# Optimization experiments

Hardware: AMD Instinct MI355X
Metric: run time of the kernel (lower is better)

Reference implementation:

```python
import jax, jax.numpy as jnp
import numpy as np

DIM = 256
HEADS = 4
B, N = 2, 4096
NEG = -1e9
EPS = 1e-5


def setup_inputs() -> dict:
    key = jax.random.key(0)
    ks = jax.random.split(key, 12)
    s = 0.02
    inp = {
        "x": jax.random.normal(ks[0], (B, N, DIM), dtype=jnp.float32),
        "adj": jax.random.randint(ks[1], (B, N, N), 0, 2, dtype=jnp.int32),
        "Wq": jax.random.normal(ks[2], (DIM, DIM), dtype=jnp.float32) * s,
        "bq": jnp.zeros((DIM,), jnp.float32),
        "Wk": jax.random.normal(ks[3], (DIM, DIM), dtype=jnp.float32) * s,
        "bk": jnp.zeros((DIM,), jnp.float32),
        "Wv": jax.random.normal(ks[4], (DIM, DIM), dtype=jnp.float32) * s,
        "bv": jnp.zeros((DIM,), jnp.float32),
        "Wo": jax.random.normal(ks[5], (DIM, DIM), dtype=jnp.float32) * s,
        "bo": jnp.zeros((DIM,), jnp.float32),
        "gamma": jnp.ones((DIM,), jnp.float32),
        "beta": jnp.zeros((DIM,), jnp.float32),
    }
    return inp


def reference(x, adj, Wq, bq, Wk, bk, Wv, bv, Wo, bo, gamma, beta):
    Bx, Nx, C = x.shape
    H = HEADS
    D = C // H
    scale = D ** (-0.5)
    # torch Linear: y = x @ W.T + b
    def proj(W, b):
        return (x @ W.T + b).reshape(Bx, Nx, H, D).transpose(0, 2, 1, 3)  # [B,H,N,D]
    q = proj(Wq, bq)
    k = proj(Wk, bk)
    v = proj(Wv, bv)
    attn = jnp.einsum("bhnd,bhmd->bhnm", q, k) * scale          # [B,H,N,N]
    attn = jnp.where(adj[:, None, :, :] == 0, NEG, attn)
    attn = jax.nn.softmax(attn, axis=-1)
    # dropout omitted (eval mode / deterministic reference)
    out = jnp.einsum("bhnm,bhmd->bhnd", attn, v)                # [B,H,N,D]
    out = out.transpose(0, 2, 1, 3).reshape(Bx, Nx, C)
    out = out @ Wo.T + bo
    mu = jnp.mean(out, axis=-1, keepdims=True)
    var = jnp.var(out, axis=-1, keepdims=True)
    return (out - mu) * jax.lax.rsqrt(var + EPS) * gamma + beta
```

## Files before the change

kernel.cpp:

```cpp
#include <hip/hip_runtime.h>
#include <stdint.h>

#define CDIM 256
#define HEADS 4
#define HD 64
#define NB 2
#define NN 4096

typedef unsigned short u16;
typedef unsigned char u8;
typedef unsigned long long u64;
typedef __attribute__((ext_vector_type(8))) short short8;
typedef __attribute__((ext_vector_type(4))) float f32x4;
typedef __attribute__((ext_vector_type(16))) float f32x16;

#define QSCALE 0.1803368801111244f

__device__ __forceinline__ u16 f2bf(float f) {
  union { float f; unsigned u; } v; v.f = f;
  return (u16)((v.u + 0x7fffu + ((v.u >> 16) & 1u)) >> 16);
}
__device__ __forceinline__ float bf2f(u16 u) {
  union { unsigned u; float f; } v; v.u = ((unsigned)u) << 16; return v.f;
}
__device__ __forceinline__ short8 fragf32(const float* p) {
  float4 a = reinterpret_cast<const float4*>(p)[0];
  float4 b = reinterpret_cast<const float4*>(p)[1];
  short8 h;
  h[0] = (short)f2bf(a.x); h[1] = (short)f2bf(a.y);
  h[2] = (short)f2bf(a.z); h[3] = (short)f2bf(a.w);
  h[4] = (short)f2bf(b.x); h[5] = (short)f2bf(b.y);
  h[6] = (short)f2bf(b.z); h[7] = (short)f2bf(b.w);
  return h;
}
__device__ __forceinline__ f32x16 zero16() {
  f32x16 z;
#pragma unroll
  for (int i = 0; i < 16; ++i) z[i] = 0.f;
  return z;
}
__device__ __forceinline__ unsigned cvt_pk_bf16(float lo, float hi) {
  unsigned r;
  asm("v_cvt_pk_bf16_f32 %0, %1, %2" : "=v"(r) : "v"(lo), "v"(hi));
  return r;
}
__device__ __forceinline__ void permlane32_swap(unsigned& a, unsigned& b) {
  asm("v_permlane32_swap_b32 %0, %1" : "+v"(a), "+v"(b));
}

__global__ __launch_bounds__(256) void prep(
    const int* __restrict__ adj, u8* __restrict__ bmb,
    const float* __restrict__ Wq, const float* __restrict__ Wk,
    const float* __restrict__ Wv, const float* __restrict__ Wo,
    u16* __restrict__ Wqb, u16* __restrict__ Wkb,
    u16* __restrict__ Wvb, u16* __restrict__ Wob) {
  const int blk = blockIdx.x;
  if (blk < 4096) {
    const int wave = threadIdx.x >> 6, lane = threadIdx.x & 63;
    const int c0 = blk * 16 + wave * 4;
#pragma unroll
    for (int it = 0; it < 4; ++it) {
      int c = c0 + it;
      int row = c >> 3, kb = (c & 7) * 512;
      const int* src = adj + (size_t)row * 4096 + kb + lane * 8;
      uint4 a = *reinterpret_cast<const uint4*>(src);
      uint4 b = *reinterpret_cast<const uint4*>(src + 4);
      unsigned byte = 0;
      byte |= (a.x != 0) ? 1u : 0u;
      byte |= (a.y != 0) ? 2u : 0u;
      byte |= (a.z != 0) ? 4u : 0u;
      byte |= (a.w != 0) ? 8u : 0u;
      byte |= (b.x != 0) ? 16u : 0u;
      byte |= (b.y != 0) ? 32u : 0u;
      byte |= (b.z != 0) ? 64u : 0u;
      byte |= (b.w != 0) ? 128u : 0u;
      bmb[(size_t)row * 512 + (c & 7) * 64 + lane] = (u8)byte;
    }
  } else {
    size_t base = ((size_t)(blk - 4096) * 256 + threadIdx.x) * 8;
    int w = (int)(base >> 16);
    size_t lo = base & 65535;
    const float* src;
    u16* dst;
    if (w == 0)      { src = Wq + lo; dst = Wqb + lo; }
    else if (w == 1) { src = Wk + lo; dst = Wkb + lo; }
    else if (w == 2) { src = Wv + lo; dst = Wvb + lo; }
    else             { src = Wo + lo; dst = Wob + lo; }
    *reinterpret_cast<short8*>(dst) = fragf32(src);
  }
}

__global__ __launch_bounds__(256) void qkv_gemm(
    const float* __restrict__ x,
    const u16* __restrict__ Wqb, const u16* __restrict__ Wkb,
    const u16* __restrict__ Wvb,
    const float* __restrict__ bq, const float* __restrict__ bk,
    const float* __restrict__ bv,
    u16* __restrict__ Qb, u16* __restrict__ Kb, u16* __restrict__ Vtb) {
  const int tid = threadIdx.x, w = tid >> 6, lane = tid & 63;
  const int quad = lane >> 4, l15 = lane & 15;
  const int tok0 = blockIdx.x * 16;
  const int b = tok0 >> 12, nl = tok0 & 4095;
  const int ym = blockIdx.y;

  f32x4 acc[4];
#pragma unroll
  for (int i = 0; i < 4; ++i) acc[i] = (f32x4){0.f, 0.f, 0.f, 0.f};

  if (ym < 2) {
    const u16* Wb = (ym == 0) ? Wqb : Wkb;
    const float* bias = (ym == 0) ? bq : bk;
    const float scale = (ym == 0) ? QSCALE : 1.0f;
    u16* outp = (ym == 0) ? Qb : Kb;
#pragma unroll
    for (int ks = 0; ks < 8; ++ks) {
      short8 af = fragf32(x + (size_t)(tok0 + l15) * 256 + ks * 32 + quad * 8);
#pragma unroll
      for (int ns = 0; ns < 4; ++ns) {
        short8 bf = *reinterpret_cast<const short8*>(
            &Wb[(size_t)(w * 64 + ns * 16 + l15) * 256 + ks * 32 + quad * 8]);
        acc[ns] = __builtin_amdgcn_mfma_f32_16x16x32_bf16(af, bf, acc[ns], 0, 0, 0);
      }
    }
#pragma unroll
    for (int ns = 0; ns < 4; ++ns) {
      int d = ns * 16 + l15;
      float bb = bias[w * 64 + d];
#pragma unroll
      for (int r = 0; r < 4; ++r) {
        int tok = nl + quad * 4 + r;
        outp[((size_t)(b * HEADS + w) * NN + tok) * HD + d] =
            f2bf((acc[ns][r] + bb) * scale);
      }
    }
  } else {
#pragma unroll
    for (int ks = 0; ks < 8; ++ks) {
      short8 xf = fragf32(x + (size_t)(tok0 + l15) * 256 + ks * 32 + quad * 8);
#pragma unroll
      for (int ms = 0; ms < 4; ++ms) {
        short8 wf = *reinterpret_cast<const short8*>(
            &Wvb[(size_t)(w * 64 + ms * 16 + l15) * 256 + ks * 32 + quad * 8]);
        acc[ms] = __builtin_amdgcn_mfma_f32_16x16x32_bf16(wf, xf, acc[ms], 0, 0, 0);
      }
    }
#pragma unroll
    for (int ms = 0; ms < 4; ++ms) {
#pragma unroll
      for (int r = 0; r < 4; ++r) {
        int d = ms * 16 + quad * 4 + r;
        float bb = bv[w * 64 + d];
        Vtb[((size_t)((b * HEADS + w) * HD + d)) * NN + nl + l15] =
            f2bf(acc[ms][r] + bb);
      }
    }
  }
}

__global__ __launch_bounds__(256) void attn_mfma(
    const u16* __restrict__ Qb, const u16* __restrict__ Kb,
    const u16* __restrict__ Vtb, const u64* __restrict__ bm,
    u16* __restrict__ Opb, float* __restrict__ Lp) {
  __shared__ __align__(16) u16 KVs[2 * 8192];

  const int tid = threadIdx.x;
  const int wave = tid >> 6, lane = tid & 63;
  const int h5 = lane >> 5, l31 = lane & 31, l7 = lane & 7;
  const int bh = blockIdx.y, b = bh >> 2, h = bh & 3;
  const int q0 = blockIdx.x * 128 + wave * 32;
  const int half = blockIdx.z;
  const int key0 = half * 2048;

  const u16* qr = Qb + ((size_t)bh * NN + q0 + l31) * HD + h5 * 8;
  const short8 qf0 = *reinterpret_cast<const short8*>(qr);
  const short8 qf1 = *reinterpret_cast<const short8*>(qr + 16);
  const short8 qf2 = *reinterpret_cast<const short8*>(qr + 32);
  const short8 qf3 = *reinterpret_cast<const short8*>(qr + 48);

  short8 ones;
#pragma unroll
  for (int i = 0; i < 8; ++i) ones[i] = (short)0x3F80;

  f32x16 Oacc0 = zero16(), Oacc1 = zero16(), Oli = zero16();

  int sdk[4];
#pragma unroll
  for (int j = 0; j < 4; ++j) sdk[j] = ((2 * j + h5) ^ l7) << 3;

  const int srow = tid >> 2;
  const int wbu0 = ((((tid & 3) * 2)     ^ (srow & 7)) << 3) + srow * 64;
  const int wbu1 = ((((tid & 3) * 2 + 1) ^ (srow & 7)) << 3) + srow * 64;

  const u16* kbase = Kb + (size_t)bh * NN * HD + (size_t)key0 * HD;
  const u16* vbase = Vtb + (size_t)bh * HD * NN + key0;
  const u64* bmr = bm + ((size_t)b * NN + q0 + l31) * 64 + half * 32;

  uint4 k0, k1, v0, v1;
  {
    const uint4* kp = reinterpret_cast<const uint4*>(kbase) + tid * 2;
    k0 = kp[0]; k1 = kp[1];
    const u16* vp = vbase + (size_t)srow * NN + (tid & 3) * 16;
    v0 = *reinterpret_cast<const uint4*>(vp);
    v1 = *reinterpret_cast<const uint4*>(vp + 8);
  }
  *reinterpret_cast<uint4*>(&KVs[wbu0]) = k0;
  *reinterpret_cast<uint4*>(&KVs[wbu1]) = k1;
  *reinterpret_cast<uint4*>(&KVs[4096 + wbu0]) = v0;
  *reinterpret_cast<uint4*>(&KVs[4096 + wbu1]) = v1;
  {
    const uint4* kp = reinterpret_cast<const uint4*>(kbase + 4096) + tid * 2;
    k0 = kp[0]; k1 = kp[1];
    const u16* vp = vbase + (size_t)srow * NN + 64 + (tid & 3) * 16;
    v0 = *reinterpret_cast<const uint4*>(vp);
    v1 = *reinterpret_cast<const uint4*>(vp + 8);
  }
  u64 amc = bmr[0];

  for (int mt = 0; mt < 32; ++mt) {
    __syncthreads();
    const u64 am = amc;
    if (mt + 1 < 32) amc = bmr[mt + 1];
    const int cb = (mt & 1) * 8192;

    f32x16 s0 = zero16(), s1 = zero16();
#pragma unroll
    for (int dk = 0; dk < 4; ++dk) {
      short8 a0 = *reinterpret_cast<const short8*>(&KVs[cb + l31 * 64 + sdk[dk]]);
      short8 a1 = *reinterpret_cast<const short8*>(&KVs[cb + 2048 + l31 * 64 + sdk[dk]]);
      const short8 qf = (dk == 0) ? qf0 : (dk == 1) ? qf1 : (dk == 2) ? qf2 : qf3;
      s0 = __builtin_amdgcn_mfma_f32_32x32x16_bf16(a0, qf, s0, 0, 0, 0);
      s1 = __builtin_amdgcn_mfma_f32_32x32x16_bf16(a1, qf, s1, 0, 0, 0);
    }

    const u64 ash = am >> (4 * h5);
    const unsigned mlo = (unsigned)ash, mhi = (unsigned)(ash >> 32);

    uint4 pf0, pf1, pf2, pf3;
    {
      float pp[16];
#pragma unroll
      for (int r = 0; r < 16; ++r) {
        const int c = (r & 3) + 8 * (r >> 2);
        pp[r] = ((mlo >> c) & 1u) ? __builtin_amdgcn_exp2f(s0[r]) : 0.f;
      }
      unsigned wAe = cvt_pk_bf16(pp[0], pp[1]),  wBe = cvt_pk_bf16(pp[2], pp[3]);
      unsigned wAo = cvt_pk_bf16(pp[4], pp[5]),  wBo = cvt_pk_bf16(pp[6], pp[7]);
      permlane32_swap(wAe, wAo);
      permlane32_swap(wBe, wBo);
      pf0 = (uint4){wAe, wBe, wAo, wBo};
      wAe = cvt_pk_bf16(pp[8], pp[9]);   wBe = cvt_pk_bf16(pp[10], pp[11]);
      wAo = cvt_pk_bf16(pp[12], pp[13]); wBo = cvt_pk_bf16(pp[14], pp[15]);
      permlane32_swap(wAe, wAo);
      permlane32_swap(wBe, wBo);
      pf1 = (uint4){wAe, wBe, wAo, wBo};
    }
    {
      float pp[16];
#pragma unroll
      for (int r = 0; r < 16; ++r) {
        const int c = (r & 3) + 8 * (r >> 2);
        pp[r] = ((mhi >> c) & 1u) ? __builtin_amdgcn_exp2f(s1[r]) : 0.f;
      }
      unsigned wAe = cvt_pk_bf16(pp[0], pp[1]),  wBe = cvt_pk_bf16(pp[2], pp[3]);
      unsigned wAo = cvt_pk_bf16(pp[4], pp[5]),  wBo = cvt_pk_bf16(pp[6], pp[7]);
      permlane32_swap(wAe, wAo);
      permlane32_swap(wBe, wBo);
      pf2 = (uint4){wAe, wBe, wAo, wBo};
      wAe = cvt_pk_bf16(pp[8], pp[9]);   wBe = cvt_pk_bf16(pp[10], pp[11]);
      wAo = cvt_pk_bf16(pp[12], pp[13]); wBo = cvt_pk_bf16(pp[14], pp[15]);
      permlane32_swap(wAe, wAo);
      permlane32_swap(wBe, wBo);
      pf3 = (uint4){wAe, wBe, wAo, wBo};
    }

#pragma unroll
    for (int kb = 0; kb < 4; ++kb) {
      union { uint4 u; short8 s; } cv;
      cv.u = (kb == 0) ? pf0 : (kb == 1) ? pf1 : (kb == 2) ? pf2 : pf3;
      const short8 pa = cv.s;
      Oli = __builtin_amdgcn_mfma_f32_32x32x16_bf16(pa, ones, Oli, 0, 0, 0);
      short8 vf0 = *reinterpret_cast<const short8*>(&KVs[cb + 4096 + l31 * 64 + sdk[kb]]);
      short8 vf1 = *reinterpret_cast<const short8*>(&KVs[cb + 6144 + l31 * 64 + sdk[kb]]);
      Oacc0 = __builtin_amdgcn_mfma_f32_32x32x16_bf16(pa, vf0, Oacc0, 0, 0, 0);
      Oacc1 = __builtin_amdgcn_mfma_f32_32x32x16_bf16(pa, vf1, Oacc1, 0, 0, 0);
    }

    if (mt + 1 < 32) {
      const int nb = ((mt + 1) & 1) * 8192;
      *reinterpret_cast<uint4*>(&KVs[nb + wbu0]) = k0;
      *reinterpret_cast<uint4*>(&KVs[nb + wbu1]) = k1;
      *reinterpret_cast<uint4*>(&KVs[nb + 4096 + wbu0]) = v0;
      *reinterpret_cast<uint4*>(&KVs[nb + 4096 + wbu1]) = v1;
      if (mt + 2 < 32) {
        const uint4* kp =
            reinterpret_cast<const uint4*>(kbase + (size_t)(mt + 2) * 4096) + tid * 2;
        k0 = kp[0]; k1 = kp[1];
        const u16* vp = vbase + (size_t)srow * NN + (mt + 2) * 64 + (tid & 3) * 16;
        v0 = *reinterpret_cast<const uint4*>(vp);
        v1 = *reinterpret_cast<const uint4*>(vp + 8);
      }
    }
  }

  u16* ob = Opb + (size_t)(half * NB + b) * NN * CDIM;
#pragma unroll
  for (int r = 0; r < 16; ++r) {
    const int tok = q0 + (r & 3) + 8 * (r >> 2) + 4 * h5;
    u16* orow = ob + (size_t)tok * CDIM + h * HD;
    orow[l31] = f2bf(Oacc0[r]);
    orow[32 + l31] = f2bf(Oacc1[r]);
    if (l31 == 0) Lp[((size_t)half * 8 + bh) * NN + tok] = Oli[r];
  }
}

__global__ __launch_bounds__(256) void comb_oproj(
    const u16* __restrict__ Opb, const float* __restrict__ Lp,
    const u16* __restrict__ Wob, const float* __restrict__ bo,
    const float* __restrict__ gamma, const float* __restrict__ beta,
    float* __restrict__ out) {
  __shared__ u16 As[16 * 264];
  __shared__ float ys[16][264];
  __shared__ float linv[64];
  const int tid = threadIdx.x, w = tid >> 6, lane = tid & 63;
  const int quad = lane >> 4, l15 = lane & 15;
  const int tok0 = blockIdx.x * 16;
  const int b = tok0 >> 12, nl = tok0 & 4095;

  if (tid < 64) {
    int tokr = tid >> 2, hh = tid & 3;
    int bh = b * 4 + hh;
    int n = nl + tokr;
    float s = Lp[(size_t)bh * NN + n] + Lp[(size_t)(8 + bh) * NN + n];
    linv[tokr * 4 + hh] = (s > 0.f) ? (1.f / s) : 0.f;
  }
  __syncthreads();

  {
    int tokr = tid >> 4, ch0 = (tid & 15) * 16;
    size_t base = ((size_t)b * NN + nl + tokr) * CDIM + ch0;
    uint4 a0 = *reinterpret_cast<const uint4*>(Opb + base);
    uint4 a1 = *reinterpret_cast<const uint4*>(Opb + base + 8);
    uint4 c0 = *reinterpret_cast<const uint4*>(Opb + 2097152 + base);
    uint4 c1 = *reinterpret_cast<const uint4*>(Opb + 2097152 + base + 8);
    float inv = linv[tokr * 4 + (ch0 >> 6)];
    unsigned wa[8] = {a0.x, a0.y, a0.z, a0.w, a1.x, a1.y, a1.z, a1.w};
    unsigned wb[8] = {c0.x, c0.y, c0.z, c0.w, c1.x, c1.y, c1.z, c1.w};
    u16 ov[16];
#pragma unroll
    for (int i = 0; i < 8; ++i) {
      float lo = (bf2f((u16)(wa[i] & 0xffffu)) + bf2f((u16)(wb[i] & 0xffffu))) * inv;
      float hi = (bf2f((u16)(wa[i] >> 16)) + bf2f((u16)(wb[i] >> 16))) * inv;
      ov[2 * i] = f2bf(lo);
      ov[2 * i + 1] = f2bf(hi);
    }
    u16* dst = &As[tokr * 264 + ch0];
    *reinterpret_cast<uint4*>(dst) = *reinterpret_cast<uint4*>(ov);
    *reinterpret_cast<uint4*>(dst + 8) = *reinterpret_cast<uint4*>(ov + 8);
  }
  __syncthreads();

  f32x4 acc[4];
#pragma unroll
  for (int i = 0; i < 4; ++i) acc[i] = (f32x4){0.f, 0.f, 0.f, 0.f};
#pragma unroll
  for (int ks = 0; ks < 8; ++ks) {
    short8 af = *reinterpret_cast<const short8*>(&As[l15 * 264 + ks * 32 + quad * 8]);
#pragma unroll
    for (int ns = 0; ns < 4; ++ns) {
      short8 bf = *reinterpret_cast<const short8*>(
          &Wob[(size_t)(w * 64 + ns * 16 + l15) * 256 + ks * 32 + quad * 8]);
      acc[ns] = __builtin_amdgcn_mfma_f32_16x16x32_bf16(af, bf, acc[ns], 0, 0, 0);
    }
  }

#pragma unroll
  for (int ns = 0; ns < 4; ++ns) {
    int ch = w * 64 + ns * 16 + l15;
    float bb = bo[ch];
#pragma unroll
    for (int r = 0; r < 4; ++r) ys[quad * 4 + r][ch] = acc[ns][r] + bb;
  }
  __syncthreads();

  float g[4], bt[4];
#pragma unroll
  for (int i = 0; i < 4; ++i) {
    g[i] = gamma[lane + i * 64];
    bt[i] = beta[lane + i * 64];
  }
#pragma unroll
  for (int rr = 0; rr < 4; ++rr) {
    int r = w * 4 + rr;
    float v[4], s = 0.f, s2 = 0.f;
#pragma unroll
    for (int i = 0; i < 4; ++i) {
      v[i] = ys[r][lane + i * 64];
      s += v[i];
      s2 = fmaf(v[i], v[i], s2);
    }
#pragma unroll
    for (int off = 32; off > 0; off >>= 1) {
      s += __shfl_xor(s, off, 64);
      s2 += __shfl_xor(s2, off, 64);
    }
    float mu = s * (1.f / 256.f);
    float rs = rsqrtf(s2 * (1.f / 256.f) - mu * mu + 1e-5f);
    float* orow = out + (size_t)(tok0 + r) * 256;
#pragma unroll
    for (int i = 0; i < 4; ++i)
      orow[lane + i * 64] = (v[i] - mu) * rs * g[i] + bt[i];
  }
}

extern "C" void kernel_launch(void* const* d_in, const int* in_sizes, int n_in,
                              void* d_out, int out_size, void* d_ws, size_t ws_size,
                              hipStream_t stream) {
  const float* x     = (const float*)d_in[0];
  const int*   adj   = (const int*)d_in[1];
  const float* Wq    = (const float*)d_in[2];
  const float* bq    = (const float*)d_in[3];
  const float* Wk    = (const float*)d_in[4];
  const float* bk    = (const float*)d_in[5];
  const float* Wv    = (const float*)d_in[6];
  const float* bv    = (const float*)d_in[7];
  const float* Wo    = (const float*)d_in[8];
  const float* bo    = (const float*)d_in[9];
  const float* gamma = (const float*)d_in[10];
  const float* beta  = (const float*)d_in[11];
  float* out = (float*)d_out;

  const size_t PER = (size_t)NB * HEADS * NN * HD;
  u16* Wqb = (u16*)d_ws;
  u16* Wkb = Wqb + 65536;
  u16* Wvb = Wkb + 65536;
  u16* Wob = Wvb + 65536;
  u64* bmp = (u64*)(Wob + 65536);
  u16* Qb  = (u16*)(bmp + 524288);
  u16* Kb  = Qb + PER;
  u16* Vtb = Kb + PER;
  u16* Opb = Vtb + PER;
  float* Lp = (float*)(Opb + 2 * PER);

  const size_t NEED = (size_t)((u16*)(Lp + 65536) - (u16*)d_ws) * sizeof(u16);
  if (ws_size < NEED) return;

  prep<<<dim3(4224), dim3(256), 0, stream>>>(
      adj, (u8*)bmp, Wq, Wk, Wv, Wo, Wqb, Wkb, Wvb, Wob);

  qkv_gemm<<<dim3(512, 3), dim3(256), 0, stream>>>(
      x, Wqb, Wkb, Wvb, bq, bk, bv, Qb, Kb, Vtb);

  attn_mfma<<<dim3(NN / 128, NB * HEADS, 2), dim3(256), 0, stream>>>(
      Qb, Kb, Vtb, bmp, Opb, Lp);

  comb_oproj<<<dim3((NB * NN) / 16), dim3(256), 0, stream>>>(
      Opb, Lp, Wob, bo, gamma, beta, out);
}
```

Before: 317.7 us.

## Split attention keys into four partitions, add wave priority hints and occupancy bound

The attention kernel now splits the key range into four chunks instead of two, which doubles the grid to 1024 blocks so the GPU's compute units are better filled. The combine kernel sums four partial outputs and row sums instead of two. The kernel also raises wave priority around the MFMA blocks and sets a minimum of three blocks per CU in the launch bounds. In exchange it doubles partial-output traffic to and from global memory and repeats the Q loads and prologue per block.

```diff
diff --git a/kernel.cpp b/kernel.cpp
--- a/kernel.cpp
+++ b/kernel.cpp
@@ -157,7 +157,7 @@
   }
 }
 
-__global__ __launch_bounds__(256) void attn_mfma(
+__global__ __launch_bounds__(256, 3) void attn_mfma(
     const u16* __restrict__ Qb, const u16* __restrict__ Kb,
     const u16* __restrict__ Vtb, const u64* __restrict__ bm,
     u16* __restrict__ Opb, float* __restrict__ Lp) {
@@ -168,8 +168,9 @@
   const int h5 = lane >> 5, l31 = lane & 31, l7 = lane & 7;
   const int bh = blockIdx.y, b = bh >> 2, h = bh & 3;
   const int q0 = blockIdx.x * 128 + wave * 32;
-  const int half = blockIdx.z;
-  const int key0 = half * 2048;
+  const int quarter = blockIdx.z;
+  const int key0 = quarter * 1024;
+  const int NT = 16;
 
   const u16* qr = Qb + ((size_t)bh * NN + q0 + l31) * HD + h5 * 8;
   const short8 qf0 = *reinterpret_cast<const short8*>(qr);
@@ -193,7 +194,7 @@
 
   const u16* kbase = Kb + (size_t)bh * NN * HD + (size_t)key0 * HD;
   const u16* vbase = Vtb + (size_t)bh * HD * NN + key0;
-  const u64* bmr = bm + ((size_t)b * NN + q0 + l31) * 64 + half * 32;
+  const u64* bmr = bm + ((size_t)b * NN + q0 + l31) * 64 + quarter * 16;
 
   uint4 k0, k1, v0, v1;
   {
@@ -216,13 +217,14 @@
   }
   u64 amc = bmr[0];
 
-  for (int mt = 0; mt < 32; ++mt) {
+  for (int mt = 0; mt < NT; ++mt) {
     __syncthreads();
     const u64 am = amc;
-    if (mt + 1 < 32) amc = bmr[mt + 1];
+    if (mt + 1 < NT) amc = bmr[mt + 1];
     const int cb = (mt & 1) * 8192;
 
     f32x16 s0 = zero16(), s1 = zero16();
+    __builtin_amdgcn_s_setprio(1);
 #pragma unroll
     for (int dk = 0; dk < 4; ++dk) {
       short8 a0 = *reinterpret_cast<const short8*>(&KVs[cb + l31 * 64 + sdk[dk]]);
@@ -231,6 +233,7 @@
       s0 = __builtin_amdgcn_mfma_f32_32x32x16_bf16(a0, qf, s0, 0, 0, 0);
       s1 = __builtin_amdgcn_mfma_f32_32x32x16_bf16(a1, qf, s1, 0, 0, 0);
     }
+    __builtin_amdgcn_s_setprio(0);
 
     const u64 ash = am >> (4 * h5);
     const unsigned mlo = (unsigned)ash, mhi = (unsigned)(ash >> 32);
@@ -273,6 +276,7 @@
       pf3 = (uint4){wAe, wBe, wAo, wBo};
     }
 
+    __builtin_amdgcn_s_setprio(1);
 #pragma unroll
     for (int kb = 0; kb < 4; ++kb) {
       union { uint4 u; short8 s; } cv;
@@ -284,14 +288,15 @@
       Oacc0 = __builtin_amdgcn_mfma_f32_32x32x16_bf16(pa, vf0, Oacc0, 0, 0, 0);
       Oacc1 = __builtin_amdgcn_mfma_f32_32x32x16_bf16(pa, vf1, Oacc1, 0, 0, 0);
     }
-
-    if (mt + 1 < 32) {
+    __builtin_amdgcn_s_setprio(0);
+
+    if (mt + 1 < NT) {
       const int nb = ((mt + 1) & 1) * 8192;
       *reinterpret_cast<uint4*>(&KVs[nb + wbu0]) = k0;
       *reinterpret_cast<uint4*>(&KVs[nb + wbu1]) = k1;
       *reinterpret_cast<uint4*>(&KVs[nb + 4096 + wbu0]) = v0;
       *reinterpret_cast<uint4*>(&KVs[nb + 4096 + wbu1]) = v1;
-      if (mt + 2 < 32) {
+      if (mt + 2 < NT) {
         const uint4* kp =
             reinterpret_cast<const uint4*>(kbase + (size_t)(mt + 2) * 4096) + tid * 2;
         k0 = kp[0]; k1 = kp[1];
@@ -302,14 +307,14 @@
     }
   }
 
-  u16* ob = Opb + (size_t)(half * NB + b) * NN * CDIM;
+  u16* ob = Opb + (size_t)(quarter * NB + b) * NN * CDIM;
 #pragma unroll
   for (int r = 0; r < 16; ++r) {
     const int tok = q0 + (r & 3) + 8 * (r >> 2) + 4 * h5;
     u16* orow = ob + (size_t)tok * CDIM + h * HD;
     orow[l31] = f2bf(Oacc0[r]);
     orow[32 + l31] = f2bf(Oacc1[r]);
-    if (l31 == 0) Lp[((size_t)half * 8 + bh) * NN + tok] = Oli[r];
+    if (l31 == 0) Lp[((size_t)quarter * 8 + bh) * NN + tok] = Oli[r];
   }
 }
 
@@ -330,7 +335,10 @@
     int tokr = tid >> 2, hh = tid & 3;
     int bh = b * 4 + hh;
     int n = nl + tokr;
-    float s = Lp[(size_t)bh * NN + n] + Lp[(size_t)(8 + bh) * NN + n];
+    float s = 0.f;
+#pragma unroll
+    for (int q = 0; q < 4; ++q)
+      s += Lp[((size_t)q * 8 + bh) * NN + n];
     linv[tokr * 4 + hh] = (s > 0.f) ? (1.f / s) : 0.f;
   }
   __syncthreads();
@@ -338,21 +346,25 @@
   {
     int tokr = tid >> 4, ch0 = (tid & 15) * 16;
     size_t base = ((size_t)b * NN + nl + tokr) * CDIM + ch0;
-    uint4 a0 = *reinterpret_cast<const uint4*>(Opb + base);
-    uint4 a1 = *reinterpret_cast<const uint4*>(Opb + base + 8);
-    uint4 c0 = *reinterpret_cast<const uint4*>(Opb + 2097152 + base);
-    uint4 c1 = *reinterpret_cast<const uint4*>(Opb + 2097152 + base + 8);
     float inv = linv[tokr * 4 + (ch0 >> 6)];
-    unsigned wa[8] = {a0.x, a0.y, a0.z, a0.w, a1.x, a1.y, a1.z, a1.w};
-    unsigned wb[8] = {c0.x, c0.y, c0.z, c0.w, c1.x, c1.y, c1.z, c1.w};
+    float acc16[16];
+#pragma unroll
+    for (int i = 0; i < 16; ++i) acc16[i] = 0.f;
+#pragma unroll
+    for (int q = 0; q < 4; ++q) {
+      size_t qb = (size_t)q * 2097152 + base;
+      uint4 a0 = *reinterpret_cast<const uint4*>(Opb + qb);
+      uint4 a1 = *reinterpret_cast<const uint4*>(Opb + qb + 8);
+      unsigned wa[8] = {a0.x, a0.y, a0.z, a0.w, a1.x, a1.y, a1.z, a1.w};
+#pragma unroll
+      for (int i = 0; i < 8; ++i) {
+        acc16[2 * i]     += bf2f((u16)(wa[i] & 0xffffu));
+        acc16[2 * i + 1] += bf2f((u16)(wa[i] >> 16));
+      }
+    }
     u16 ov[16];
 #pragma unroll
-    for (int i = 0; i < 8; ++i) {
-      float lo = (bf2f((u16)(wa[i] & 0xffffu)) + bf2f((u16)(wb[i] & 0xffffu))) * inv;
-      float hi = (bf2f((u16)(wa[i] >> 16)) + bf2f((u16)(wb[i] >> 16))) * inv;
-      ov[2 * i] = f2bf(lo);
-      ov[2 * i + 1] = f2bf(hi);
-    }
+    for (int i = 0; i < 16; ++i) ov[i] = f2bf(acc16[i] * inv);
     u16* dst = &As[tokr * 264 + ch0];
     *reinterpret_cast<uint4*>(dst) = *reinterpret_cast<uint4*>(ov);
     *reinterpret_cast<uint4*>(dst + 8) = *reinterpret_cast<uint4*>(ov + 8);
@@ -439,9 +451,9 @@
   u16* Kb  = Qb + PER;
   u16* Vtb = Kb + PER;
   u16* Opb = Vtb + PER;
-  float* Lp = (float*)(Opb + 2 * PER);
-
-  const size_t NEED = (size_t)((u16*)(Lp + 65536) - (u16*)d_ws) * sizeof(u16);
+  float* Lp = (float*)(Opb + 4 * PER);
+
+  const size_t NEED = (size_t)((u16*)(Lp + 131072) - (u16*)d_ws) * sizeof(u16);
   if (ws_size < NEED) return;
 
   prep<<<dim3(4224), dim3(256), 0, stream>>>(
@@ -450,7 +462,7 @@
   qkv_gemm<<<dim3(512, 3), dim3(256), 0, stream>>>(
       x, Wqb, Wkb, Wvb, bq, bk, bv, Qb, Kb, Vtb);
 
-  attn_mfma<<<dim3(NN / 128, NB * HEADS, 2), dim3(256), 0, stream>>>(
+  attn_mfma<<<dim3(NN / 128, NB * HEADS, 4), dim3(256), 0, stream>>>(
       Qb, Kb, Vtb, bmp, Opb, Lp);
 
   comb_oproj<<<dim3((NB * NN) / 16), dim3(256), 0, stream>>>(
```

Result: faster. 309.9 us (-2.5%).

## Software-pipeline attention: overlap QK^T of next tile with softmax and PV of previous

Applied to the files above, without the earlier changes.

Restructures the attention main loop so each iteration issues the QK^T MFMAs for the current key tile while computing exp/pack and PV MFMAs for the previous tile, using ping-pong score registers and a 2-deep K buffer with a 3-deep V ring in LDS. It adds s_setprio around the PV MFMAs and launch_bounds(256,2). The aim is to hide the VALU softmax work and LDS latency behind matrix instructions, at the cost of more registers, more LDS and more complex buffer indexing.

```diff
diff --git a/kernel.cpp b/kernel.cpp
--- a/kernel.cpp
+++ b/kernel.cpp
@@ -46,6 +46,25 @@
 }
 __device__ __forceinline__ void permlane32_swap(unsigned& a, unsigned& b) {
   asm("v_permlane32_swap_b32 %0, %1" : "+v"(a), "+v"(b));
+}
+__device__ __forceinline__ void smax_half(const f32x16& s, unsigned m32,
+                                          uint4& pfa, uint4& pfb) {
+  float pp[16];
+#pragma unroll
+  for (int r = 0; r < 16; ++r) {
+    const int c = (r & 3) + 8 * (r >> 2);
+    pp[r] = ((m32 >> c) & 1u) ? __builtin_amdgcn_exp2f(s[r]) : 0.f;
+  }
+  unsigned wAe = cvt_pk_bf16(pp[0], pp[1]),  wBe = cvt_pk_bf16(pp[2], pp[3]);
+  unsigned wAo = cvt_pk_bf16(pp[4], pp[5]),  wBo = cvt_pk_bf16(pp[6], pp[7]);
+  permlane32_swap(wAe, wAo);
+  permlane32_swap(wBe, wBo);
+  pfa = (uint4){wAe, wBe, wAo, wBo};
+  wAe = cvt_pk_bf16(pp[8], pp[9]);   wBe = cvt_pk_bf16(pp[10], pp[11]);
+  wAo = cvt_pk_bf16(pp[12], pp[13]); wBo = cvt_pk_bf16(pp[14], pp[15]);
+  permlane32_swap(wAe, wAo);
+  permlane32_swap(wBe, wBo);
+  pfb = (uint4){wAe, wBe, wAo, wBo};
 }
 
 __global__ __launch_bounds__(256) void prep(
@@ -157,11 +176,65 @@
   }
 }
 
-__global__ __launch_bounds__(256) void attn_mfma(
+#define QKT_DK(A0, A1, QF, SD)                                                 \
+  { short8 ka_ = *reinterpret_cast<const short8*>(&KVs[k_p0 + l31 * 64 + SD]); \
+    short8 kc_ =                                                               \
+        *reinterpret_cast<const short8*>(&KVs[k_p0 + 2048 + l31 * 64 + SD]);   \
+    A0 = __builtin_amdgcn_mfma_f32_32x32x16_bf16(ka_, QF, A0, 0, 0, 0);        \
+    A1 = __builtin_amdgcn_mfma_f32_32x32x16_bf16(kc_, QF, A1, 0, 0, 0); }
+
+#define PV_KB(PF, SD)                                                          \
+  { union { uint4 u; short8 s; } cv_; cv_.u = PF;                              \
+    const short8 pa_ = cv_.s;                                                  \
+    Oli = __builtin_amdgcn_mfma_f32_32x32x16_bf16(pa_, ones, Oli, 0, 0, 0);    \
+    short8 vf0_ =                                                              \
+        *reinterpret_cast<const short8*>(&KVs[v_pm1 + l31 * 64 + SD]);         \
+    short8 vf1_ =                                                              \
+        *reinterpret_cast<const short8*>(&KVs[v_pm1 + 2048 + l31 * 64 + SD]);  \
+    Oacc0 = __builtin_amdgcn_mfma_f32_32x32x16_bf16(pa_, vf0_, Oacc0, 0, 0, 0);\
+    Oacc1 = __builtin_amdgcn_mfma_f32_32x32x16_bf16(pa_, vf1_, Oacc1, 0, 0, 0); }
+
+#define BODY(A0, A1, B0, B1, PT, MI, LOADM, DOPREV)                            \
+  {                                                                            \
+    __syncthreads();                                                           \
+    *reinterpret_cast<uint4*>(&KVs[k_pp1 + wbu0]) = k0;                        \
+    *reinterpret_cast<uint4*>(&KVs[k_pp1 + wbu1]) = k1;                        \
+    *reinterpret_cast<uint4*>(&KVs[v_pp1 + wbu0]) = v0;                        \
+    *reinterpret_cast<uint4*>(&KVs[v_pp1 + wbu1]) = v1;                        \
+    { const uint4* kp_ =                                                       \
+          reinterpret_cast<const uint4*>(kbase + (size_t)(PT) * 4096) + tid*2; \
+      k0 = kp_[0]; k1 = kp_[1];                                                \
+      const u16* vp_ = vbase + (size_t)srow * NN + (PT) * 64 + (tid & 3) * 16; \
+      v0 = *reinterpret_cast<const uint4*>(vp_);                               \
+      v1 = *reinterpret_cast<const uint4*>(vp_ + 8); }                         \
+    const u64 ash_ = am_prev >> (4 * h5);                                      \
+    A0 = zero16(); A1 = zero16();                                              \
+    QKT_DK(A0, A1, qf0, sdk[0]);                                               \
+    QKT_DK(A0, A1, qf1, sdk[1]);                                               \
+    uint4 pf0, pf1, pf2, pf3;                                                  \
+    if (DOPREV) smax_half(B0, (unsigned)ash_, pf0, pf1);                       \
+    QKT_DK(A0, A1, qf2, sdk[2]);                                               \
+    QKT_DK(A0, A1, qf3, sdk[3]);                                               \
+    if (DOPREV) smax_half(B1, (unsigned)(ash_ >> 32), pf2, pf3);               \
+    if (DOPREV) {                                                              \
+      __builtin_amdgcn_s_setprio(1);                                           \
+      PV_KB(pf0, sdk[0]);                                                      \
+      PV_KB(pf1, sdk[1]);                                                      \
+      PV_KB(pf2, sdk[2]);                                                      \
+      PV_KB(pf3, sdk[3]);                                                      \
+      __builtin_amdgcn_s_setprio(0);                                           \
+    }                                                                          \
+    k_p0 ^= 4096; k_pp1 ^= 4096;                                               \
+    { int tv_ = v_pm1; v_pm1 = v_p0; v_p0 = v_pp1; v_pp1 = tv_; }              \
+    am_prev = am_cur;                                                          \
+    if (LOADM) am_cur = bmr[MI];                                               \
+  }
+
+__global__ __launch_bounds__(256, 2) void attn_mfma(
     const u16* __restrict__ Qb, const u16* __restrict__ Kb,
     const u16* __restrict__ Vtb, const u64* __restrict__ bm,
     u16* __restrict__ Opb, float* __restrict__ Lp) {
-  __shared__ __align__(16) u16 KVs[2 * 8192];
+  __shared__ __align__(16) u16 KVs[5 * 4096];
 
   const int tid = threadIdx.x;
   const int wave = tid >> 6, lane = tid & 63;
@@ -182,6 +255,7 @@
   for (int i = 0; i < 8; ++i) ones[i] = (short)0x3F80;
 
   f32x16 Oacc0 = zero16(), Oacc1 = zero16(), Oli = zero16();
+  f32x16 sX0, sX1, sY0, sY1;
 
   int sdk[4];
 #pragma unroll
@@ -194,6 +268,9 @@
   const u16* kbase = Kb + (size_t)bh * NN * HD + (size_t)key0 * HD;
   const u16* vbase = Vtb + (size_t)bh * HD * NN + key0;
   const u64* bmr = bm + ((size_t)b * NN + q0 + l31) * 64 + half * 32;
+
+  int k_p0 = 0, k_pp1 = 4096;
+  int v_pm1 = 8192 + 8192, v_p0 = 8192, v_pp1 = 8192 + 4096;
 
   uint4 k0, k1, v0, v1;
   {
@@ -202,11 +279,11 @@
     const u16* vp = vbase + (size_t)srow * NN + (tid & 3) * 16;
     v0 = *reinterpret_cast<const uint4*>(vp);
     v1 = *reinterpret_cast<const uint4*>(vp + 8);
-  }
-  *reinterpret_cast<uint4*>(&KVs[wbu0]) = k0;
-  *reinterpret_cast<uint4*>(&KVs[wbu1]) = k1;
-  *reinterpret_cast<uint4*>(&KVs[4096 + wbu0]) = v0;
-  *reinterpret_cast<uint4*>(&KVs[4096 + wbu1]) = v1;
+    *reinterpret_cast<uint4*>(&KVs[wbu0]) = k0;
+    *reinterpret_cast<uint4*>(&KVs[wbu1]) = k1;
+    *reinterpret_cast<uint4*>(&KVs[8192 + wbu0]) = v0;
+    *reinterpret_cast<uint4*>(&KVs[8192 + wbu1]) = v1;
+  }
   {
     const uint4* kp = reinterpret_cast<const uint4*>(kbase + 4096) + tid * 2;
     k0 = kp[0]; k1 = kp[1];
@@ -214,92 +291,25 @@
     v0 = *reinterpret_cast<const uint4*>(vp);
     v1 = *reinterpret_cast<const uint4*>(vp + 8);
   }
-  u64 amc = bmr[0];
-
-  for (int mt = 0; mt < 32; ++mt) {
-    __syncthreads();
-    const u64 am = amc;
-    if (mt + 1 < 32) amc = bmr[mt + 1];
-    const int cb = (mt & 1) * 8192;
-
-    f32x16 s0 = zero16(), s1 = zero16();
-#pragma unroll
-    for (int dk = 0; dk < 4; ++dk) {
-      short8 a0 = *reinterpret_cast<const short8*>(&KVs[cb + l31 * 64 + sdk[dk]]);
-      short8 a1 = *reinterpret_cast<const short8*>(&KVs[cb + 2048 + l31 * 64 + sdk[dk]]);
-      const short8 qf = (dk == 0) ? qf0 : (dk == 1) ? qf1 : (dk == 2) ? qf2 : qf3;
-      s0 = __builtin_amdgcn_mfma_f32_32x32x16_bf16(a0, qf, s0, 0, 0, 0);
-      s1 = __builtin_amdgcn_mfma_f32_32x32x16_bf16(a1, qf, s1, 0, 0, 0);
-    }
-
-    const u64 ash = am >> (4 * h5);
-    const unsigned mlo = (unsigned)ash, mhi = (unsigned)(ash >> 32);
-
+  u64 am_prev = 0, am_cur = bmr[0];
+
+  BODY(sX0, sX1, sY0, sY1, 2, 1, 1, 0);
+  for (int t = 1; t < 31; t += 2) {
+    BODY(sY0, sY1, sX0, sX1, t + 2, t + 1, 1, 1);
+    BODY(sX0, sX1, sY0, sY1, (t + 3 < 32 ? t + 3 : 31), t + 2, 1, 1);
+  }
+  BODY(sY0, sY1, sX0, sX1, 31, 31, 0, 1);
+  {
+    const u64 ash_ = am_prev >> (4 * h5);
     uint4 pf0, pf1, pf2, pf3;
-    {
-      float pp[16];
-#pragma unroll
-      for (int r = 0; r < 16; ++r) {
-        const int c = (r & 3) + 8 * (r >> 2);
-        pp[r] = ((mlo >> c) & 1u) ? __builtin_amdgcn_exp2f(s0[r]) : 0.f;
-      }
-      unsigned wAe = cvt_pk_bf16(pp[0], pp[1]),  wBe = cvt_pk_bf16(pp[2], pp[3]);
-      unsigned wAo = cvt_pk_bf16(pp[4], pp[5]),  wBo = cvt_pk_bf16(pp[6], pp[7]);
-      permlane32_swap(wAe, wAo);
-      permlane32_swap(wBe, wBo);
-      pf0 = (uint4){wAe, wBe, wAo, wBo};
-      wAe = cvt_pk_bf16(pp[8], pp[9]);   wBe = cvt_pk_bf16(pp[10], pp[11]);
-      wAo = cvt_pk_bf16(pp[12], pp[13]); wBo = cvt_pk_bf16(pp[14], pp[15]);
-      permlane32_swap(wAe, wAo);
-      permlane32_swap(wBe, wBo);
-      pf1 = (uint4){wAe, wBe, wAo, wBo};
-    }
-    {
-      float pp[16];
-#pragma unroll
-      for (int r = 0; r < 16; ++r) {
-        const int c = (r & 3) + 8 * (r >> 2);
-        pp[r] = ((mhi >> c) & 1u) ? __builtin_amdgcn_exp2f(s1[r]) : 0.f;
-      }
-      unsigned wAe = cvt_pk_bf16(pp[0], pp[1]),  wBe = cvt_pk_bf16(pp[2], pp[3]);
-      unsigned wAo = cvt_pk_bf16(pp[4], pp[5]),  wBo = cvt_pk_bf16(pp[6], pp[7]);
-      permlane32_swap(wAe, wAo);
-      permlane32_swap(wBe, wBo);
-      pf2 = (uint4){wAe, wBe, wAo, wBo};
-      wAe = cvt_pk_bf16(pp[8], pp[9]);   wBe = cvt_pk_bf16(pp[10], pp[11]);
-      wAo = cvt_pk_bf16(pp[12], pp[13]); wBo = cvt_pk_bf16(pp[14], pp[15]);
-      permlane32_swap(wAe, wAo);
-      permlane32_swap(wBe, wBo);
-      pf3 = (uint4){wAe, wBe, wAo, wBo};
-    }
-
-#pragma unroll
-    for (int kb = 0; kb < 4; ++kb) {
-      union { uint4 u; short8 s; } cv;
-      cv.u = (kb == 0) ? pf0 : (kb == 1) ? pf1 : (kb == 2) ? pf2 : pf3;
-      const short8 pa = cv.s;
-      Oli = __builtin_amdgcn_mfma_f32_32x32x16_bf16(pa, ones, Oli, 0, 0, 0);
-      short8 vf0 = *reinterpret_cast<const short8*>(&KVs[cb + 4096 + l31 * 64 + sdk[kb]]);
-      short8 vf1 = *reinterpret_cast<const short8*>(&KVs[cb + 6144 + l31 * 64 + sdk[kb]]);
-      Oacc0 = __builtin_amdgcn_mfma_f32_32x32x16_bf16(pa, vf0, Oacc0, 0, 0, 0);
-      Oacc1 = __builtin_amdgcn_mfma_f32_32x32x16_bf16(pa, vf1, Oacc1, 0, 0, 0);
-    }
-
-    if (mt + 1 < 32) {
-      const int nb = ((mt + 1) & 1) * 8192;
-      *reinterpret_cast<uint4*>(&KVs[nb + wbu0]) = k0;
-      *reinterpret_cast<uint4*>(&KVs[nb + wbu1]) = k1;
-      *reinterpret_cast<uint4*>(&KVs[nb + 4096 + wbu0]) = v0;
-      *reinterpret_cast<uint4*>(&KVs[nb + 4096 + wbu1]) = v1;
-      if (mt + 2 < 32) {
-        const uint4* kp =
-            reinterpret_cast<const uint4*>(kbase + (size_t)(mt + 2) * 4096) + tid * 2;
-        k0 = kp[0]; k1 = kp[1];
-        const u16* vp = vbase + (size_t)srow * NN + (mt + 2) * 64 + (tid & 3) * 16;
-        v0 = *reinterpret_cast<const uint4*>(vp);
-        v1 = *reinterpret_cast<const uint4*>(vp + 8);
-      }
-    }
+    smax_half(sY0, (unsigned)ash_, pf0, pf1);
+    smax_half(sY1, (unsigned)(ash_ >> 32), pf2, pf3);
+    __builtin_amdgcn_s_setprio(1);
+    PV_KB(pf0, sdk[0]);
+    PV_KB(pf1, sdk[1]);
+    PV_KB(pf2, sdk[2]);
+    PV_KB(pf3, sdk[3]);
+    __builtin_amdgcn_s_setprio(0);
   }
 
   u16* ob = Opb + (size_t)(half * NB + b) * NN * CDIM;
```

New measurement: 307.9 us. 3.1% less time.
